# Kernel tuning notes

Measured on AMD Instinct MI355X. Metric: run time of the kernel, lower is better.

Reference implementation:

```python
import jax, jax.numpy as jnp
import numpy as np

FREQ_RES = 100.0 / 256.0
NUM_FILTERS = 6
_CFG = [(0.5, 4.0), (4.0, 8.0), (8.0, 12.0), (12.0, 16.0), (16.0, 24.0), (24.0, 30.0)]
BANDS = [(int(a / FREQ_RES), int(b / FREQ_RES)) for a, b in _CFG]  # (start_bin, end_bin)


def _interp_idx(n_src, n_dst):
    # torch F.interpolate bilinear, align_corners=False, along last dim (T dim is identity since same size)
    j = np.arange(n_dst)
    src = np.maximum((j + 0.5) * n_src / n_dst - 0.5, 0.0)
    x0 = np.floor(src).astype(np.int32)
    x1 = np.minimum(x0 + 1, n_src - 1)
    w = (src - x0).astype(np.float32)
    return x0, x1, w


def _gelu(x):
    return jax.nn.gelu(x, approximate=False)


def _forward(spec, centers, widths, gains, align_w, align_b, fc1_w, fc1_b, fc2_w, fc2_b,
             band_gain, gate_w, gate_b, proj_w, proj_b, bn_gamma, bn_beta, bn_mean, bn_var):
    B, C, T, F = spec.shape
    N = NUM_FILTERS
    band_feats = []
    for i, (s, e) in enumerate(BANDS):
        nb = e - s + 1
        sl = spec[:, :, :, s:e + 1]                       # [B,C,T,nb]
        mu = jax.nn.softplus(centers[i]) + s              # [C,N]
        mu = jnp.clip(mu, s, s + nb - 1)
        std = jnp.clip(jax.nn.softplus(widths[i]) + 1e-3, 0.5, 2.0 * nb / N)
        freqs = jnp.arange(nb, dtype=spec.dtype)          # relative bins [nb]
        g = jnp.exp(-0.5 * ((freqs[None, None, :] - mu[:, :, None]) / std[:, :, None]) ** 2)  # [C,N,nb]
        w = gains[i][:, :, None] * g / (g.sum(-1, keepdims=True) + 1e-6)
        filt = jnp.einsum('bctf,cnf->bctn', sl, w)        # [B,C,T,N]
        aligned = jnp.einsum('bctn,dc->bdtn', filt, align_w[i]) + align_b[i][None, :, None, None]
        band_feats.append(aligned)
    band_stack = jnp.stack(band_feats, axis=1)            # [B,6,C,T,N]
    nb_bands = band_stack.shape[1]
    x = band_stack.reshape(B, nb_bands * C, T, N)
    h = _gelu(jnp.einsum('bktn,ok->botn', x, fc1_w) + fc1_b[None, :, None, None])
    attn = jnp.einsum('botn,ko->bktn', h, fc2_w) + fc2_b[None, :, None, None]
    attn = jax.nn.softmax(attn.reshape(B, nb_bands, C, T, N), axis=1)  # softmax over bands
    band_stack = band_stack * attn * band_gain[None, :, None, None, None]
    enhanced = jnp.zeros_like(spec)
    for i, (s, e) in enumerate(BANDS):
        nb = e - s + 1
        narrow = band_stack[:, i]                         # [B,C,T,N]
        x0, x1, wl = _interp_idx(NUM_FILTERS, nb)
        wl = jnp.asarray(wl, dtype=spec.dtype)
        bf = narrow[..., x0] * (1.0 - wl) + narrow[..., x1] * wl   # [B,C,T,nb]
        enhanced = enhanced.at[:, :, :, s:e + 1].add(bf)
    residual = enhanced - spec
    gate = jax.nn.sigmoid(jnp.einsum('bctf,dc->bdtf', residual, gate_w) + gate_b[None, :, None, None])
    enhanced2 = spec + gate * residual
    y = jnp.einsum('bctf,dc->bdtf', enhanced2, proj_w) + proj_b[None, :, None, None]
    y = (y - bn_mean[None, :, None, None]) / jnp.sqrt(bn_var[None, :, None, None] + 1e-5)
    y = y * bn_gamma[None, :, None, None] + bn_beta[None, :, None, None]
    return _gelu(y)


def setup_inputs() -> dict:
    key = jax.random.key(0)
    ks = jax.random.split(key, 8)
    B, C, T, F, N = 64, 3, 3000, 103, NUM_FILTERS
    spec = jax.random.normal(ks[0], (B, C, T, F), dtype=jnp.float32)
    centers = jnp.stack([jnp.broadcast_to(jnp.linspace(a, b, N, dtype=jnp.float32) / FREQ_RES, (C, N)) for a, b in _CFG])
    widths = jnp.stack([jnp.full((C, N), (b - a) / N / FREQ_RES, dtype=jnp.float32) for a, b in _CFG])
    gains = jnp.ones((6, C, N), jnp.float32)
    align_w = jax.random.normal(ks[1], (6, C, C), dtype=jnp.float32) / np.sqrt(C)
    align_b = jax.random.normal(ks[2], (6, C), dtype=jnp.float32) * 0.02
    inter = 2 * C
    fc1_w = jax.random.normal(ks[3], (inter, 6 * C), dtype=jnp.float32) / np.sqrt(6 * C)
    fc1_b = jnp.zeros((inter,), jnp.float32)
    fc2_w = jax.random.normal(ks[4], (6 * C, inter), dtype=jnp.float32) / np.sqrt(inter)
    fc2_b = jnp.zeros((6 * C,), jnp.float32)
    band_gain = jnp.ones((6,), jnp.float32)
    gate_w = jax.random.normal(ks[5], (C, C), dtype=jnp.float32) / np.sqrt(C)
    gate_b = jnp.zeros((C,), jnp.float32)
    proj_w = jax.random.normal(ks[6], (C, C), dtype=jnp.float32) / np.sqrt(C)
    proj_b = jnp.zeros((C,), jnp.float32)
    bn_gamma = jnp.ones((C,), jnp.float32)
    bn_beta = jnp.zeros((C,), jnp.float32)
    bn_mean = jnp.zeros((C,), jnp.float32)
    bn_var = jnp.ones((C,), jnp.float32)
    return {"spec": spec, "centers": centers, "widths": widths, "gains": gains,
            "align_w": align_w, "align_b": align_b, "fc1_w": fc1_w, "fc1_b": fc1_b,
            "fc2_w": fc2_w, "fc2_b": fc2_b, "band_gain": band_gain,
            "gate_w": gate_w, "gate_b": gate_b, "proj_w": proj_w, "proj_b": proj_b,
            "bn_gamma": bn_gamma, "bn_beta": bn_beta, "bn_mean": bn_mean, "bn_var": bn_var}


def reference(spec, centers, widths, gains, align_w, align_b, fc1_w, fc1_b, fc2_w, fc2_b,
              band_gain, gate_w, gate_b, proj_w, proj_b, bn_gamma, bn_beta, bn_mean, bn_var):
    return _forward(spec, centers, widths, gains, align_w, align_b, fc1_w, fc1_b, fc2_w, fc2_b,
                    band_gain, gate_w, gate_b, proj_w, proj_b, bn_gamma, bn_beta, bn_mean, bn_var)
```

## Files before the change

### kernel.cpp

```cpp
#include <hip/hip_runtime.h>
#include <math.h>

namespace {

constexpr int C_ = 3, T_ = 3000, F_ = 103, NB_ = 6;
constexpr int TT = 20;
constexpr int BS[NB_]  = {1, 10, 20, 30, 40, 61};
constexpr int BNB[NB_] = {10, 11, 11, 11, 22, 16};
constexpr int BOF[NB_] = {0, 10, 21, 32, 43, 65};
constexpr int SPF = 81;
constexpr int PLANE = T_ * F_;
constexpr int SECP = 2064;
constexpr int POOLN = 6320;

__device__ __forceinline__ float softplus_(float x) {
  return fmaxf(x, 0.0f) + log1pf(expf(-fabsf(x)));
}
__device__ __forceinline__ float sigmoid_(float z) {
  return 1.0f / (1.0f + __expf(-z));
}
__device__ __forceinline__ float gelu_(float x) {
  return x * sigmoid_(1.595769122f * x * (1.0f + 0.044715f * x * x));
}

__global__ __launch_bounds__(256)
void sleepband_kernel(const float* __restrict__ spec,
                      const float* __restrict__ centers,
                      const float* __restrict__ widths,
                      const float* __restrict__ gains,
                      const float* __restrict__ align_w,
                      const float* __restrict__ align_b,
                      const float* __restrict__ fc1_w,
                      const float* __restrict__ fc1_b,
                      const float* __restrict__ fc2_w,
                      const float* __restrict__ fc2_b,
                      const float* __restrict__ band_gain,
                      const float* __restrict__ gate_w,
                      const float* __restrict__ gate_b,
                      const float* __restrict__ proj_w,
                      const float* __restrict__ proj_b,
                      const float* __restrict__ bn_gamma,
                      const float* __restrict__ bn_beta,
                      const float* __restrict__ bn_mean,
                      const float* __restrict__ bn_var,
                      float* __restrict__ out)
{
  __shared__ __align__(16) float sPool[POOLN];
  __shared__ float sBand[TT][109];
  __shared__ float sAw[54], sAb[18], sF1[108], sF1b[6], sF2[108], sF2b[18],
                   sBg[6], sGw[9], sGb[3], sPw[9], sPb[3];

  const int tid = threadIdx.x;
  const int t0  = blockIdx.x * TT;
  const int b   = blockIdx.y;

  float* sW = sPool + C_ * TT * SPF;

  const float* specB = spec + (size_t)b * C_ * PLANE;
  for (int li = tid; li < C_ * TT * SPF; li += 256) {
    int c   = li / (TT * SPF);
    int rem = li - c * (TT * SPF);
    int tt  = rem / SPF;
    int f   = rem - tt * SPF;
    sPool[li] = specB[(size_t)c * PLANE + (size_t)(t0 + tt) * F_ + f];
  }

  const float* sp0 = specB + (size_t)t0 * F_;
  const int e1 = tid * 4;
  const int e2 = e1 + 1024;
  const float4 pA1 = *(const float4*)(sp0 + e1);
  const float4 pB1 = *(const float4*)(sp0 + PLANE + e1);
  const float4 pC1 = *(const float4*)(sp0 + 2 * PLANE + e1);
  const float4 pA2 = *(const float4*)(sp0 + e2);
  const float4 pB2 = *(const float4*)(sp0 + PLANE + e2);
  const float4 pC2 = *(const float4*)(sp0 + 2 * PLANE + e2);
  float4 pA3 = {0,0,0,0}, pB3 = {0,0,0,0}, pC3 = {0,0,0,0};
  const int e3 = 2048 + tid * 4;
  if (tid < 3) {
    pA3 = *(const float4*)(sp0 + e3);
    pB3 = *(const float4*)(sp0 + PLANE + e3);
    pC3 = *(const float4*)(sp0 + 2 * PLANE + e3);
  }

  if (tid < 54)  sAw[tid]  = align_w[tid];
  if (tid < 18)  sAb[tid]  = align_b[tid];
  if (tid < 108) sF1[tid]  = fc1_w[tid];
  if (tid < 6)   sF1b[tid] = fc1_b[tid];
  if (tid < 108) sF2[tid]  = fc2_w[tid];
  if (tid < 18)  sF2b[tid] = fc2_b[tid];
  if (tid < 6)   sBg[tid]  = band_gain[tid];
  if (tid < 9)   sGw[tid]  = gate_w[tid];
  if (tid < 3)   sGb[tid]  = gate_b[tid];
  if (tid < 9) {
    int d = tid / 3;
    float sc = bn_gamma[d] / sqrtf(bn_var[d] + 1e-5f);
    sPw[tid] = proj_w[tid] * sc;
  }
  if (tid < 3) {
    float sc = bn_gamma[tid] / sqrtf(bn_var[tid] + 1e-5f);
    sPb[tid] = (proj_b[tid] - bn_mean[tid]) * sc + bn_beta[tid];
  }

  if (tid >= 128 && tid < 128 + 108) {
    int q = tid - 128;
    int i = q / 18;
    int p = q - i * 18;
    int s = BS[i], nb = BNB[i];
    float mu = softplus_(centers[q]) + (float)s;
    mu = fminf(fmaxf(mu, (float)s), (float)(s + nb - 1));
    float sd = softplus_(widths[q]) + 0.001f;
    sd = fminf(fmaxf(sd, 0.5f), 2.0f * (float)nb / 6.0f);
    float sum = 0.0f;
    for (int f = 0; f < nb; ++f) {
      float d = ((float)f - mu) / sd;
      sum += __expf(-0.5f * d * d);
    }
    float sc = gains[q] / (sum + 1e-6f);
    float* wrow = &sW[BOF[i] * 18 + p * nb];
    for (int f = 0; f < nb; ++f) {
      float d = ((float)f - mu) / sd;
      wrow[f] = sc * __expf(-0.5f * d * d);
    }
  }
  __syncthreads();

  for (int task = tid; task < 18 * TT; task += 256) {
    int p  = task / TT;
    int tt = task - p * TT;
    int c  = p / 6;
    int n  = p - c * 6;
    const float* srowb = &sPool[(c * TT + tt) * SPF];
    #pragma unroll
    for (int i = 0; i < NB_; ++i) {
      const float* wrow = &sW[BOF[i] * 18 + p * BNB[i]];
      const float* srow = srowb + BS[i];
      float acc = 0.0f;
      #pragma unroll
      for (int f = 0; f < BNB[i]; ++f) acc += srow[f] * wrow[f];
      sBand[tt][(i * 3 + c) * 6 + n] = acc;
    }
  }
  __syncthreads();

  if (tid < 6 * TT) {
    int n  = tid / TT;
    int tt = tid - n * TT;
    float al[18];
    #pragma unroll
    for (int i = 0; i < 6; ++i) {
      float f0 = sBand[tt][(i * 3 + 0) * 6 + n];
      float f1 = sBand[tt][(i * 3 + 1) * 6 + n];
      float f2 = sBand[tt][(i * 3 + 2) * 6 + n];
      #pragma unroll
      for (int d = 0; d < 3; ++d)
        al[i * 3 + d] = sAw[i * 9 + d * 3 + 0] * f0 + sAw[i * 9 + d * 3 + 1] * f1 +
                        sAw[i * 9 + d * 3 + 2] * f2 + sAb[i * 3 + d];
    }
    float h[6];
    #pragma unroll
    for (int o = 0; o < 6; ++o) {
      float acc = sF1b[o];
      #pragma unroll
      for (int k = 0; k < 18; ++k) acc += sF1[o * 18 + k] * al[k];
      h[o] = gelu_(acc);
    }
    float at[18];
    #pragma unroll
    for (int k = 0; k < 18; ++k) {
      float acc = sF2b[k];
      #pragma unroll
      for (int o = 0; o < 6; ++o) acc += sF2[k * 6 + o] * h[o];
      at[k] = acc;
    }
    #pragma unroll
    for (int c = 0; c < 3; ++c) {
      float m = at[c];
      #pragma unroll
      for (int i = 1; i < 6; ++i) m = fmaxf(m, at[i * 3 + c]);
      float e[6], ssum = 0.0f;
      #pragma unroll
      for (int i = 0; i < 6; ++i) { e[i] = __expf(at[i * 3 + c] - m); ssum += e[i]; }
      float inv = 1.0f / ssum;
      #pragma unroll
      for (int i = 0; i < 6; ++i)
        sBand[tt][(i * 3 + c) * 6 + n] = al[i * 3 + c] * (e[i] * inv) * sBg[i];
    }
  }
  __syncthreads();

  if (tid < C_ * TT) {
    const int c  = tid / TT;
    const int tt = tid - c * TT;
    float bnd[36];
    #pragma unroll
    for (int i = 0; i < 6; ++i)
      #pragma unroll
      for (int n = 0; n < 6; ++n)
        bnd[i * 6 + n] = sBand[tt][(i * 3 + c) * 6 + n];
    float* row = &sPool[c * SECP + tt * F_];
    row[0] = 0.0f;
    float carry = 0.0f;
    #pragma unroll
    for (int i = 0; i < NB_; ++i) {
      #pragma unroll
      for (int j = 0; j < BNB[i]; ++j) {
        float src = ((float)j + 0.5f) * 6.0f / (float)BNB[i] - 0.5f;
        src = src > 0.0f ? src : 0.0f;
        int   x0 = (int)src;
        int   x1 = (x0 < 5) ? x0 + 1 : 5;
        float wl = src - (float)x0;
        float v  = bnd[i * 6 + x0] * (1.0f - wl) + bnd[i * 6 + x1] * wl;
        if (j == 0) v += carry;
        if (i < NB_ - 1 && j == BNB[i] - 1) carry = v;
        else row[BS[i] + j] = v;
      }
    }
    #pragma unroll
    for (int f = 77; f < F_; ++f) row[f] = 0.0f;
  }
  __syncthreads();

  float gw[9], pw[9], gb3[3], pb3[3];
  #pragma unroll
  for (int k = 0; k < 9; ++k) { gw[k] = sGw[k]; pw[k] = sPw[k]; }
  #pragma unroll
  for (int k = 0; k < 3; ++k) { gb3[k] = sGb[k]; pb3[k] = sPb[k]; }

  float* outB = out + (size_t)b * C_ * PLANE + (size_t)t0 * F_;

  auto fin = [&](int e, const float4& sA, const float4& sB, const float4& sC) {
    const float4 eA = *(const float4*)&sPool[0 * SECP + e];
    const float4 eB = *(const float4*)&sPool[1 * SECP + e];
    const float4 eC = *(const float4*)&sPool[2 * SECP + e];
    float4 oA, oB, oC;
    const float* sAp = (const float*)&sA; const float* sBp = (const float*)&sB;
    const float* sCp = (const float*)&sC;
    const float* eAp = (const float*)&eA; const float* eBp = (const float*)&eB;
    const float* eCp = (const float*)&eC;
    float* oAp = (float*)&oA; float* oBp = (float*)&oB; float* oCp = (float*)&oC;
    #pragma unroll
    for (int j = 0; j < 4; ++j) {
      float sv0 = sAp[j], sv1 = sBp[j], sv2 = sCp[j];
      float r0 = eAp[j] - sv0, r1 = eBp[j] - sv1, r2 = eCp[j] - sv2;
      float e20 = sv0 + sigmoid_(gw[0] * r0 + gw[1] * r1 + gw[2] * r2 + gb3[0]) * r0;
      float e21 = sv1 + sigmoid_(gw[3] * r0 + gw[4] * r1 + gw[5] * r2 + gb3[1]) * r1;
      float e22 = sv2 + sigmoid_(gw[6] * r0 + gw[7] * r1 + gw[8] * r2 + gb3[2]) * r2;
      float y0 = pw[0] * e20 + pw[1] * e21 + pw[2] * e22 + pb3[0];
      float y1 = pw[3] * e20 + pw[4] * e21 + pw[5] * e22 + pb3[1];
      float y2 = pw[6] * e20 + pw[7] * e21 + pw[8] * e22 + pb3[2];
      oAp[j] = gelu_(y0); oBp[j] = gelu_(y1); oCp[j] = gelu_(y2);
    }
    *(float4*)(outB + e) = oA;
    *(float4*)(outB + PLANE + e) = oB;
    *(float4*)(outB + 2 * PLANE + e) = oC;
  };

  fin(e1, pA1, pB1, pC1);
  fin(e2, pA2, pB2, pC2);
  if (tid < 3) fin(e3, pA3, pB3, pC3);
}

}

extern "C" void kernel_launch(void* const* d_in, const int* in_sizes, int n_in,
                              void* d_out, int out_size, void* d_ws, size_t ws_size,
                              hipStream_t stream) {
  (void)n_in; (void)out_size; (void)d_ws; (void)ws_size;
  const int B = in_sizes[0] / (C_ * T_ * F_);
  dim3 grid(T_ / TT, B);
  sleepband_kernel<<<grid, 256, 0, stream>>>(
      (const float*)d_in[0],  (const float*)d_in[1],  (const float*)d_in[2],
      (const float*)d_in[3],  (const float*)d_in[4],  (const float*)d_in[5],
      (const float*)d_in[6],  (const float*)d_in[7],  (const float*)d_in[8],
      (const float*)d_in[9],  (const float*)d_in[10], (const float*)d_in[11],
      (const float*)d_in[12], (const float*)d_in[13], (const float*)d_in[14],
      (const float*)d_in[15], (const float*)d_in[16], (const float*)d_in[17],
      (const float*)d_in[18], (float*)d_out);
}
```

Baseline: 254.5 us.

## Cut register pressure: defer spec reloads, coarsen filter and MLP stages, raise occupancy

Drops the early float4 prefetch of the spec tile into registers and instead reloads spec from global memory inside a loop in the final gate/projection stage. This shortens register live ranges across the middle stages. The filter stage now has each thread compute three filter outputs from one shared spectrum read, and the attention MLP stage has each thread process two time steps so shared weight loads are reused. Launch bounds request 4 blocks per CU. The trade-off is that the final stage now waits on a global load that was previously overlapped, and fewer threads are active in the middle stages.

```diff
diff --git a/kernel.cpp b/kernel.cpp
--- a/kernel.cpp
+++ b/kernel.cpp
@@ -23,7 +23,7 @@
   return x * sigmoid_(1.595769122f * x * (1.0f + 0.044715f * x * x));
 }
 
-__global__ __launch_bounds__(256)
+__global__ __launch_bounds__(256, 4)
 void sleepband_kernel(const float* __restrict__ spec,
                       const float* __restrict__ centers,
                       const float* __restrict__ widths,
@@ -65,23 +65,6 @@
     sPool[li] = specB[(size_t)c * PLANE + (size_t)(t0 + tt) * F_ + f];
   }
 
-  const float* sp0 = specB + (size_t)t0 * F_;
-  const int e1 = tid * 4;
-  const int e2 = e1 + 1024;
-  const float4 pA1 = *(const float4*)(sp0 + e1);
-  const float4 pB1 = *(const float4*)(sp0 + PLANE + e1);
-  const float4 pC1 = *(const float4*)(sp0 + 2 * PLANE + e1);
-  const float4 pA2 = *(const float4*)(sp0 + e2);
-  const float4 pB2 = *(const float4*)(sp0 + PLANE + e2);
-  const float4 pC2 = *(const float4*)(sp0 + 2 * PLANE + e2);
-  float4 pA3 = {0,0,0,0}, pB3 = {0,0,0,0}, pC3 = {0,0,0,0};
-  const int e3 = 2048 + tid * 4;
-  if (tid < 3) {
-    pA3 = *(const float4*)(sp0 + e3);
-    pB3 = *(const float4*)(sp0 + PLANE + e3);
-    pC3 = *(const float4*)(sp0 + 2 * PLANE + e3);
-  }
-
   if (tid < 54)  sAw[tid]  = align_w[tid];
   if (tid < 18)  sAb[tid]  = align_b[tid];
   if (tid < 108) sF1[tid]  = fc1_w[tid];
@@ -124,66 +107,102 @@
   }
   __syncthreads();
 
-  for (int task = tid; task < 18 * TT; task += 256) {
-    int p  = task / TT;
-    int tt = task - p * TT;
-    int c  = p / 6;
-    int n  = p - c * 6;
-    const float* srowb = &sPool[(c * TT + tt) * SPF];
-    #pragma unroll
-    for (int i = 0; i < NB_; ++i) {
-      const float* wrow = &sW[BOF[i] * 18 + p * BNB[i]];
-      const float* srow = srowb + BS[i];
-      float acc = 0.0f;
-      #pragma unroll
-      for (int f = 0; f < BNB[i]; ++f) acc += srow[f] * wrow[f];
-      sBand[tt][(i * 3 + c) * 6 + n] = acc;
+  {
+    const int ng  = tid >> 6;
+    const int idx = tid & 63;
+    if (ng < 2 && idx < 60) {
+      const int c  = idx / 20;
+      const int tt = idx - c * 20;
+      const int n0 = ng * 3;
+      const float* srowb = &sPool[(c * TT + tt) * SPF];
+      #pragma unroll
+      for (int i = 0; i < NB_; ++i) {
+        const int nb = BNB[i];
+        const float* w0 = &sW[BOF[i] * 18 + (c * 6 + n0) * nb];
+        const float* sr = srowb + BS[i];
+        float a0 = 0.0f, a1 = 0.0f, a2 = 0.0f;
+        #pragma unroll
+        for (int f = 0; f < nb; ++f) {
+          float s = sr[f];
+          a0 += s * w0[f];
+          a1 += s * w0[nb + f];
+          a2 += s * w0[2 * nb + f];
+        }
+        sBand[tt][(i * 3 + c) * 6 + n0 + 0] = a0;
+        sBand[tt][(i * 3 + c) * 6 + n0 + 1] = a1;
+        sBand[tt][(i * 3 + c) * 6 + n0 + 2] = a2;
+      }
     }
   }
   __syncthreads();
 
-  if (tid < 6 * TT) {
-    int n  = tid / TT;
-    int tt = tid - n * TT;
-    float al[18];
+  if (tid < 60) {
+    const int n   = tid / 10;
+    const int tth = tid - n * 10;
+    const int tA  = 2 * tth, tB = tA + 1;
+    float al0[18], al1[18];
     #pragma unroll
     for (int i = 0; i < 6; ++i) {
-      float f0 = sBand[tt][(i * 3 + 0) * 6 + n];
-      float f1 = sBand[tt][(i * 3 + 1) * 6 + n];
-      float f2 = sBand[tt][(i * 3 + 2) * 6 + n];
-      #pragma unroll
-      for (int d = 0; d < 3; ++d)
-        al[i * 3 + d] = sAw[i * 9 + d * 3 + 0] * f0 + sAw[i * 9 + d * 3 + 1] * f1 +
-                        sAw[i * 9 + d * 3 + 2] * f2 + sAb[i * 3 + d];
-    }
-    float h[6];
+      float f00 = sBand[tA][(i * 3 + 0) * 6 + n];
+      float f01 = sBand[tA][(i * 3 + 1) * 6 + n];
+      float f02 = sBand[tA][(i * 3 + 2) * 6 + n];
+      float f10 = sBand[tB][(i * 3 + 0) * 6 + n];
+      float f11 = sBand[tB][(i * 3 + 1) * 6 + n];
+      float f12 = sBand[tB][(i * 3 + 2) * 6 + n];
+      #pragma unroll
+      for (int d = 0; d < 3; ++d) {
+        float w0 = sAw[i * 9 + d * 3 + 0];
+        float w1 = sAw[i * 9 + d * 3 + 1];
+        float w2 = sAw[i * 9 + d * 3 + 2];
+        float bb = sAb[i * 3 + d];
+        al0[i * 3 + d] = w0 * f00 + w1 * f01 + w2 * f02 + bb;
+        al1[i * 3 + d] = w0 * f10 + w1 * f11 + w2 * f12 + bb;
+      }
+    }
+    float h0[6], h1[6];
     #pragma unroll
     for (int o = 0; o < 6; ++o) {
-      float acc = sF1b[o];
-      #pragma unroll
-      for (int k = 0; k < 18; ++k) acc += sF1[o * 18 + k] * al[k];
-      h[o] = gelu_(acc);
-    }
-    float at[18];
-    #pragma unroll
-    for (int k = 0; k < 18; ++k) {
-      float acc = sF2b[k];
-      #pragma unroll
-      for (int o = 0; o < 6; ++o) acc += sF2[k * 6 + o] * h[o];
-      at[k] = acc;
+      float a0 = sF1b[o], a1 = sF1b[o];
+      #pragma unroll
+      for (int k = 0; k < 18; ++k) {
+        float w = sF1[o * 18 + k];
+        a0 += w * al0[k];
+        a1 += w * al1[k];
+      }
+      h0[o] = gelu_(a0);
+      h1[o] = gelu_(a1);
     }
     #pragma unroll
     for (int c = 0; c < 3; ++c) {
-      float m = at[c];
-      #pragma unroll
-      for (int i = 1; i < 6; ++i) m = fmaxf(m, at[i * 3 + c]);
-      float e[6], ssum = 0.0f;
-      #pragma unroll
-      for (int i = 0; i < 6; ++i) { e[i] = __expf(at[i * 3 + c] - m); ssum += e[i]; }
-      float inv = 1.0f / ssum;
-      #pragma unroll
-      for (int i = 0; i < 6; ++i)
-        sBand[tt][(i * 3 + c) * 6 + n] = al[i * 3 + c] * (e[i] * inv) * sBg[i];
+      float a0[6], a1[6];
+      #pragma unroll
+      for (int i = 0; i < 6; ++i) {
+        const int k = i * 3 + c;
+        float x0 = sF2b[k], x1 = sF2b[k];
+        #pragma unroll
+        for (int o = 0; o < 6; ++o) {
+          float w = sF2[k * 6 + o];
+          x0 += w * h0[o];
+          x1 += w * h1[o];
+        }
+        a0[i] = x0; a1[i] = x1;
+      }
+      float m0 = a0[0], m1 = a1[0];
+      #pragma unroll
+      for (int i = 1; i < 6; ++i) { m0 = fmaxf(m0, a0[i]); m1 = fmaxf(m1, a1[i]); }
+      float e0[6], e1[6], s0 = 0.0f, s1 = 0.0f;
+      #pragma unroll
+      for (int i = 0; i < 6; ++i) {
+        e0[i] = __expf(a0[i] - m0); s0 += e0[i];
+        e1[i] = __expf(a1[i] - m1); s1 += e1[i];
+      }
+      float i0 = 1.0f / s0, i1 = 1.0f / s1;
+      #pragma unroll
+      for (int i = 0; i < 6; ++i) {
+        float bg = sBg[i];
+        sBand[tA][(i * 3 + c) * 6 + n] = al0[i * 3 + c] * (e0[i] * i0) * bg;
+        sBand[tB][(i * 3 + c) * 6 + n] = al1[i * 3 + c] * (e1[i] * i1) * bg;
+      }
     }
   }
   __syncthreads();
@@ -226,9 +245,15 @@
   #pragma unroll
   for (int k = 0; k < 3; ++k) { gb3[k] = sGb[k]; pb3[k] = sPb[k]; }
 
+  const float* sp0 = specB + (size_t)t0 * F_;
   float* outB = out + (size_t)b * C_ * PLANE + (size_t)t0 * F_;
-
-  auto fin = [&](int e, const float4& sA, const float4& sB, const float4& sC) {
+  for (int e4 = tid; e4 < (TT * F_) / 4 + 1; e4 += 256) {
+    if (e4 >= (TT * F_ + 3) / 4) break;
+    const int e = e4 * 4;
+    if (e >= TT * F_) break;
+    const float4 sA = *(const float4*)(sp0 + e);
+    const float4 sB = *(const float4*)(sp0 + PLANE + e);
+    const float4 sC = *(const float4*)(sp0 + 2 * PLANE + e);
     const float4 eA = *(const float4*)&sPool[0 * SECP + e];
     const float4 eB = *(const float4*)&sPool[1 * SECP + e];
     const float4 eC = *(const float4*)&sPool[2 * SECP + e];
@@ -253,11 +278,7 @@
     *(float4*)(outB + e) = oA;
     *(float4*)(outB + PLANE + e) = oB;
     *(float4*)(outB + 2 * PLANE + e) = oC;
-  };
-
-  fin(e1, pA1, pB1, pC1);
-  fin(e2, pA2, pB2, pC2);
-  if (tid < 3) fin(e3, pA3, pB3, pC3);
+  }
 }
 
 }
```

After: 265.7 us. 4.4% more time.

## Hoist filter-weight prep into separate kernel and loop blocks over multiple time tiles

Applied to the files above, without the earlier changes.

Gaussian filter weights and BN-folded projection parameters are now computed once by a small prep kernel into workspace, rather than recomputed by every block. Each main block then handles NT consecutive time tiles in a loop, which amortises the parameter loads over more work and cuts the grid size by NT. The trade-offs are an extra kernel launch, fewer blocks (and so possibly lower occupancy or poor load balance across CUs), and losing the early prefetch of the residual spec values, which are now loaded inside the serialized per-tile loop.

```diff
diff --git a/kernel.cpp b/kernel.cpp
--- a/kernel.cpp
+++ b/kernel.cpp
@@ -5,13 +5,15 @@
 
 constexpr int C_ = 3, T_ = 3000, F_ = 103, NB_ = 6;
 constexpr int TT = 20;
+constexpr int NT = 5;
 constexpr int BS[NB_]  = {1, 10, 20, 30, 40, 61};
 constexpr int BNB[NB_] = {10, 11, 11, 11, 22, 16};
 constexpr int BOF[NB_] = {0, 10, 21, 32, 43, 65};
 constexpr int SPF = 81;
 constexpr int PLANE = T_ * F_;
 constexpr int SECP = 2064;
-constexpr int POOLN = 6320;
+constexpr int WTOT = 1458;
+constexpr int POOL2 = 6192;
 
 __device__ __forceinline__ float softplus_(float x) {
   return fmaxf(x, 0.0f) + log1pf(expf(-fabsf(x)));
@@ -23,86 +25,20 @@
   return x * sigmoid_(1.595769122f * x * (1.0f + 0.044715f * x * x));
 }
 
-__global__ __launch_bounds__(256)
-void sleepband_kernel(const float* __restrict__ spec,
-                      const float* __restrict__ centers,
-                      const float* __restrict__ widths,
-                      const float* __restrict__ gains,
-                      const float* __restrict__ align_w,
-                      const float* __restrict__ align_b,
-                      const float* __restrict__ fc1_w,
-                      const float* __restrict__ fc1_b,
-                      const float* __restrict__ fc2_w,
-                      const float* __restrict__ fc2_b,
-                      const float* __restrict__ band_gain,
-                      const float* __restrict__ gate_w,
-                      const float* __restrict__ gate_b,
-                      const float* __restrict__ proj_w,
-                      const float* __restrict__ proj_b,
-                      const float* __restrict__ bn_gamma,
-                      const float* __restrict__ bn_beta,
-                      const float* __restrict__ bn_mean,
-                      const float* __restrict__ bn_var,
-                      float* __restrict__ out)
+__global__ __launch_bounds__(128)
+void prep_kernel(const float* __restrict__ centers,
+                 const float* __restrict__ widths,
+                 const float* __restrict__ gains,
+                 const float* __restrict__ proj_w,
+                 const float* __restrict__ proj_b,
+                 const float* __restrict__ bn_gamma,
+                 const float* __restrict__ bn_beta,
+                 const float* __restrict__ bn_mean,
+                 const float* __restrict__ bn_var,
+                 float* __restrict__ ws)
 {
-  __shared__ __align__(16) float sPool[POOLN];
-  __shared__ float sBand[TT][109];
-  __shared__ float sAw[54], sAb[18], sF1[108], sF1b[6], sF2[108], sF2b[18],
-                   sBg[6], sGw[9], sGb[3], sPw[9], sPb[3];
-
-  const int tid = threadIdx.x;
-  const int t0  = blockIdx.x * TT;
-  const int b   = blockIdx.y;
-
-  float* sW = sPool + C_ * TT * SPF;
-
-  const float* specB = spec + (size_t)b * C_ * PLANE;
-  for (int li = tid; li < C_ * TT * SPF; li += 256) {
-    int c   = li / (TT * SPF);
-    int rem = li - c * (TT * SPF);
-    int tt  = rem / SPF;
-    int f   = rem - tt * SPF;
-    sPool[li] = specB[(size_t)c * PLANE + (size_t)(t0 + tt) * F_ + f];
-  }
-
-  const float* sp0 = specB + (size_t)t0 * F_;
-  const int e1 = tid * 4;
-  const int e2 = e1 + 1024;
-  const float4 pA1 = *(const float4*)(sp0 + e1);
-  const float4 pB1 = *(const float4*)(sp0 + PLANE + e1);
-  const float4 pC1 = *(const float4*)(sp0 + 2 * PLANE + e1);
-  const float4 pA2 = *(const float4*)(sp0 + e2);
-  const float4 pB2 = *(const float4*)(sp0 + PLANE + e2);
-  const float4 pC2 = *(const float4*)(sp0 + 2 * PLANE + e2);
-  float4 pA3 = {0,0,0,0}, pB3 = {0,0,0,0}, pC3 = {0,0,0,0};
-  const int e3 = 2048 + tid * 4;
-  if (tid < 3) {
-    pA3 = *(const float4*)(sp0 + e3);
-    pB3 = *(const float4*)(sp0 + PLANE + e3);
-    pC3 = *(const float4*)(sp0 + 2 * PLANE + e3);
-  }
-
-  if (tid < 54)  sAw[tid]  = align_w[tid];
-  if (tid < 18)  sAb[tid]  = align_b[tid];
-  if (tid < 108) sF1[tid]  = fc1_w[tid];
-  if (tid < 6)   sF1b[tid] = fc1_b[tid];
-  if (tid < 108) sF2[tid]  = fc2_w[tid];
-  if (tid < 18)  sF2b[tid] = fc2_b[tid];
-  if (tid < 6)   sBg[tid]  = band_gain[tid];
-  if (tid < 9)   sGw[tid]  = gate_w[tid];
-  if (tid < 3)   sGb[tid]  = gate_b[tid];
-  if (tid < 9) {
-    int d = tid / 3;
-    float sc = bn_gamma[d] / sqrtf(bn_var[d] + 1e-5f);
-    sPw[tid] = proj_w[tid] * sc;
-  }
-  if (tid < 3) {
-    float sc = bn_gamma[tid] / sqrtf(bn_var[tid] + 1e-5f);
-    sPb[tid] = (proj_b[tid] - bn_mean[tid]) * sc + bn_beta[tid];
-  }
-
-  if (tid >= 128 && tid < 128 + 108) {
-    int q = tid - 128;
+  const int q = threadIdx.x;
+  if (q < 108) {
     int i = q / 18;
     int p = q - i * 18;
     int s = BS[i], nb = BNB[i];
@@ -116,148 +52,208 @@
       sum += __expf(-0.5f * d * d);
     }
     float sc = gains[q] / (sum + 1e-6f);
-    float* wrow = &sW[BOF[i] * 18 + p * nb];
+    float* wrow = &ws[BOF[i] * 18 + p * nb];
     for (int f = 0; f < nb; ++f) {
       float d = ((float)f - mu) / sd;
       wrow[f] = sc * __expf(-0.5f * d * d);
     }
+  } else if (q < 117) {
+    int k = q - 108, d = k / 3;
+    float sc = bn_gamma[d] / sqrtf(bn_var[d] + 1e-5f);
+    ws[WTOT + k] = proj_w[k] * sc;
+  } else if (q < 120) {
+    int d = q - 117;
+    float sc = bn_gamma[d] / sqrtf(bn_var[d] + 1e-5f);
+    ws[WTOT + 9 + d] = (proj_b[d] - bn_mean[d]) * sc + bn_beta[d];
   }
-  __syncthreads();
-
-  for (int task = tid; task < 18 * TT; task += 256) {
-    int p  = task / TT;
-    int tt = task - p * TT;
-    int c  = p / 6;
-    int n  = p - c * 6;
-    const float* srowb = &sPool[(c * TT + tt) * SPF];
+}
+
+__global__ __launch_bounds__(256)
+void sleepband_kernel(const float* __restrict__ spec,
+                      const float* __restrict__ ws,
+                      const float* __restrict__ align_w,
+                      const float* __restrict__ align_b,
+                      const float* __restrict__ fc1_w,
+                      const float* __restrict__ fc1_b,
+                      const float* __restrict__ fc2_w,
+                      const float* __restrict__ fc2_b,
+                      const float* __restrict__ band_gain,
+                      const float* __restrict__ gate_w,
+                      const float* __restrict__ gate_b,
+                      float* __restrict__ out)
+{
+  __shared__ __align__(16) float sPool[POOL2];
+  __shared__ float sW[WTOT];
+  __shared__ float sBand[TT][109];
+  __shared__ float sAw[54], sAb[18], sF1[108], sF1b[6], sF2[108], sF2b[18],
+                   sBg[6], sGw[9], sGb[3], sPw[9], sPb[3];
+
+  const int tid = threadIdx.x;
+  const int b   = blockIdx.y;
+  const float* specB = spec + (size_t)b * C_ * PLANE;
+  float* outBase = out + (size_t)b * C_ * PLANE;
+
+  for (int k = tid; k < WTOT; k += 256) sW[k] = ws[k];
+  if (tid < 54)  sAw[tid]  = align_w[tid];
+  if (tid < 18)  sAb[tid]  = align_b[tid];
+  if (tid < 108) sF1[tid]  = fc1_w[tid];
+  if (tid < 6)   sF1b[tid] = fc1_b[tid];
+  if (tid < 108) sF2[tid]  = fc2_w[tid];
+  if (tid < 18)  sF2b[tid] = fc2_b[tid];
+  if (tid < 6)   sBg[tid]  = band_gain[tid];
+  if (tid < 9)   sGw[tid]  = gate_w[tid];
+  if (tid < 3)   sGb[tid]  = gate_b[tid];
+  if (tid < 9)   sPw[tid]  = ws[WTOT + tid];
+  if (tid < 3)   sPb[tid]  = ws[WTOT + 9 + tid];
+
+  for (int tile = 0; tile < NT; ++tile) {
+    const int t0 = (blockIdx.x * NT + tile) * TT;
+
+    for (int li = tid; li < C_ * TT * SPF; li += 256) {
+      int c   = li / (TT * SPF);
+      int rem = li - c * (TT * SPF);
+      int tt  = rem / SPF;
+      int f   = rem - tt * SPF;
+      sPool[li] = specB[(size_t)c * PLANE + (size_t)(t0 + tt) * F_ + f];
+    }
+    __syncthreads();
+
+    for (int task = tid; task < 18 * TT; task += 256) {
+      int p  = task / TT;
+      int tt = task - p * TT;
+      int c  = p / 6;
+      int n  = p - c * 6;
+      const float* srowb = &sPool[(c * TT + tt) * SPF];
+      #pragma unroll
+      for (int i = 0; i < NB_; ++i) {
+        const float* wrow = &sW[BOF[i] * 18 + p * BNB[i]];
+        const float* srow = srowb + BS[i];
+        float acc = 0.0f;
+        #pragma unroll
+        for (int f = 0; f < BNB[i]; ++f) acc += srow[f] * wrow[f];
+        sBand[tt][(i * 3 + c) * 6 + n] = acc;
+      }
+    }
+    __syncthreads();
+
+    if (tid < 6 * TT) {
+      int n  = tid / TT;
+      int tt = tid - n * TT;
+      float al[18];
+      #pragma unroll
+      for (int i = 0; i < 6; ++i) {
+        float f0 = sBand[tt][(i * 3 + 0) * 6 + n];
+        float f1 = sBand[tt][(i * 3 + 1) * 6 + n];
+        float f2 = sBand[tt][(i * 3 + 2) * 6 + n];
+        #pragma unroll
+        for (int d = 0; d < 3; ++d)
+          al[i * 3 + d] = sAw[i * 9 + d * 3 + 0] * f0 + sAw[i * 9 + d * 3 + 1] * f1 +
+                          sAw[i * 9 + d * 3 + 2] * f2 + sAb[i * 3 + d];
+      }
+      float h[6];
+      #pragma unroll
+      for (int o = 0; o < 6; ++o) {
+        float acc = sF1b[o];
+        #pragma unroll
+        for (int k = 0; k < 18; ++k) acc += sF1[o * 18 + k] * al[k];
+        h[o] = gelu_(acc);
+      }
+      float at[18];
+      #pragma unroll
+      for (int k = 0; k < 18; ++k) {
+        float acc = sF2b[k];
+        #pragma unroll
+        for (int o = 0; o < 6; ++o) acc += sF2[k * 6 + o] * h[o];
+        at[k] = acc;
+      }
+      #pragma unroll
+      for (int c = 0; c < 3; ++c) {
+        float m = at[c];
+        #pragma unroll
+        for (int i = 1; i < 6; ++i) m = fmaxf(m, at[i * 3 + c]);
+        float e[6], ssum = 0.0f;
+        #pragma unroll
+        for (int i = 0; i < 6; ++i) { e[i] = __expf(at[i * 3 + c] - m); ssum += e[i]; }
+        float inv = 1.0f / ssum;
+        #pragma unroll
+        for (int i = 0; i < 6; ++i)
+          sBand[tt][(i * 3 + c) * 6 + n] = al[i * 3 + c] * (e[i] * inv) * sBg[i];
+      }
+    }
+    __syncthreads();
+
+    if (tid < C_ * TT) {
+      const int c  = tid / TT;
+      const int tt = tid - c * TT;
+      float bnd[36];
+      #pragma unroll
+      for (int i = 0; i < 6; ++i)
+        #pragma unroll
+        for (int n = 0; n < 6; ++n)
+          bnd[i * 6 + n] = sBand[tt][(i * 3 + c) * 6 + n];
+      float* row = &sPool[c * SECP + tt * F_];
+      row[0] = 0.0f;
+      float carry = 0.0f;
+      #pragma unroll
+      for (int i = 0; i < NB_; ++i) {
+        #pragma unroll
+        for (int j = 0; j < BNB[i]; ++j) {
+          float src = ((float)j + 0.5f) * 6.0f / (float)BNB[i] - 0.5f;
+          src = src > 0.0f ? src : 0.0f;
+          int   x0 = (int)src;
+          int   x1 = (x0 < 5) ? x0 + 1 : 5;
+          float wl = src - (float)x0;
+          float v  = bnd[i * 6 + x0] * (1.0f - wl) + bnd[i * 6 + x1] * wl;
+          if (j == 0) v += carry;
+          if (i < NB_ - 1 && j == BNB[i] - 1) carry = v;
+          else row[BS[i] + j] = v;
+        }
+      }
+      #pragma unroll
+      for (int f = 77; f < F_; ++f) row[f] = 0.0f;
+    }
+    __syncthreads();
+
+    float gw[9], pw[9], gb3[3], pb3[3];
     #pragma unroll
-    for (int i = 0; i < NB_; ++i) {
-      const float* wrow = &sW[BOF[i] * 18 + p * BNB[i]];
-      const float* srow = srowb + BS[i];
-      float acc = 0.0f;
-      #pragma unroll
-      for (int f = 0; f < BNB[i]; ++f) acc += srow[f] * wrow[f];
-      sBand[tt][(i * 3 + c) * 6 + n] = acc;
-    }
+    for (int k = 0; k < 9; ++k) { gw[k] = sGw[k]; pw[k] = sPw[k]; }
+    #pragma unroll
+    for (int k = 0; k < 3; ++k) { gb3[k] = sGb[k]; pb3[k] = sPb[k]; }
+
+    const float* sp0 = specB + (size_t)t0 * F_;
+    float* outB = outBase + (size_t)t0 * F_;
+    for (int e4 = tid; e4 < (TT * F_) / 4; e4 += 256) {
+      const int e = e4 * 4;
+      const float4 sA = *(const float4*)(sp0 + e);
+      const float4 sB = *(const float4*)(sp0 + PLANE + e);
+      const float4 sC = *(const float4*)(sp0 + 2 * PLANE + e);
+      const float4 eA = *(const float4*)&sPool[0 * SECP + e];
+      const float4 eB = *(const float4*)&sPool[1 * SECP + e];
+      const float4 eC = *(const float4*)&sPool[2 * SECP + e];
+      float4 oA, oB, oC;
+      const float* sAp = (const float*)&sA; const float* sBp = (const float*)&sB;
+      const float* sCp = (const float*)&sC;
+      const float* eAp = (const float*)&eA; const float* eBp = (const float*)&eB;
+      const float* eCp = (const float*)&eC;
+      float* oAp = (float*)&oA; float* oBp = (float*)&oB; float* oCp = (float*)&oC;
+      #pragma unroll
+      for (int j = 0; j < 4; ++j) {
+        float sv0 = sAp[j], sv1 = sBp[j], sv2 = sCp[j];
+        float r0 = eAp[j] - sv0, r1 = eBp[j] - sv1, r2 = eCp[j] - sv2;
+        float e20 = sv0 + sigmoid_(gw[0] * r0 + gw[1] * r1 + gw[2] * r2 + gb3[0]) * r0;
+        float e21 = sv1 + sigmoid_(gw[3] * r0 + gw[4] * r1 + gw[5] * r2 + gb3[1]) * r1;
+        float e22 = sv2 + sigmoid_(gw[6] * r0 + gw[7] * r1 + gw[8] * r2 + gb3[2]) * r2;
+        float y0 = pw[0] * e20 + pw[1] * e21 + pw[2] * e22 + pb3[0];
+        float y1 = pw[3] * e20 + pw[4] * e21 + pw[5] * e22 + pb3[1];
+        float y2 = pw[6] * e20 + pw[7] * e21 + pw[8] * e22 + pb3[2];
+        oAp[j] = gelu_(y0); oBp[j] = gelu_(y1); oCp[j] = gelu_(y2);
+      }
+      *(float4*)(outB + e) = oA;
+      *(float4*)(outB + PLANE + e) = oB;
+      *(float4*)(outB + 2 * PLANE + e) = oC;
+    }
+    __syncthreads();
   }
-  __syncthreads();
-
-  if (tid < 6 * TT) {
-    int n  = tid / TT;
-    int tt = tid - n * TT;
-    float al[18];
-    #pragma unroll
-    for (int i = 0; i < 6; ++i) {
-      float f0 = sBand[tt][(i * 3 + 0) * 6 + n];
-      float f1 = sBand[tt][(i * 3 + 1) * 6 + n];
-      float f2 = sBand[tt][(i * 3 + 2) * 6 + n];
-      #pragma unroll
-      for (int d = 0; d < 3; ++d)
-        al[i * 3 + d] = sAw[i * 9 + d * 3 + 0] * f0 + sAw[i * 9 + d * 3 + 1] * f1 +
-                        sAw[i * 9 + d * 3 + 2] * f2 + sAb[i * 3 + d];
-    }
-    float h[6];
-    #pragma unroll
-    for (int o = 0; o < 6; ++o) {
-      float acc = sF1b[o];
-      #pragma unroll
-      for (int k = 0; k < 18; ++k) acc += sF1[o * 18 + k] * al[k];
-      h[o] = gelu_(acc);
-    }
-    float at[18];
-    #pragma unroll
-    for (int k = 0; k < 18; ++k) {
-      float acc = sF2b[k];
-      #pragma unroll
-      for (int o = 0; o < 6; ++o) acc += sF2[k * 6 + o] * h[o];
-      at[k] = acc;
-    }
-    #pragma unroll
-    for (int c = 0; c < 3; ++c) {
-      float m = at[c];
-      #pragma unroll
-      for (int i = 1; i < 6; ++i) m = fmaxf(m, at[i * 3 + c]);
-      float e[6], ssum = 0.0f;
-      #pragma unroll
-      for (int i = 0; i < 6; ++i) { e[i] = __expf(at[i * 3 + c] - m); ssum += e[i]; }
-      float inv = 1.0f / ssum;
-      #pragma unroll
-      for (int i = 0; i < 6; ++i)
-        sBand[tt][(i * 3 + c) * 6 + n] = al[i * 3 + c] * (e[i] * inv) * sBg[i];
-    }
-  }
-  __syncthreads();
-
-  if (tid < C_ * TT) {
-    const int c  = tid / TT;
-    const int tt = tid - c * TT;
-    float bnd[36];
-    #pragma unroll
-    for (int i = 0; i < 6; ++i)
-      #pragma unroll
-      for (int n = 0; n < 6; ++n)
-        bnd[i * 6 + n] = sBand[tt][(i * 3 + c) * 6 + n];
-    float* row = &sPool[c * SECP + tt * F_];
-    row[0] = 0.0f;
-    float carry = 0.0f;
-    #pragma unroll
-    for (int i = 0; i < NB_; ++i) {
-      #pragma unroll
-      for (int j = 0; j < BNB[i]; ++j) {
-        float src = ((float)j + 0.5f) * 6.0f / (float)BNB[i] - 0.5f;
-        src = src > 0.0f ? src : 0.0f;
-        int   x0 = (int)src;
-        int   x1 = (x0 < 5) ? x0 + 1 : 5;
-        float wl = src - (float)x0;
-        float v  = bnd[i * 6 + x0] * (1.0f - wl) + bnd[i * 6 + x1] * wl;
-        if (j == 0) v += carry;
-        if (i < NB_ - 1 && j == BNB[i] - 1) carry = v;
-        else row[BS[i] + j] = v;
-      }
-    }
-    #pragma unroll
-    for (int f = 77; f < F_; ++f) row[f] = 0.0f;
-  }
-  __syncthreads();
-
-  float gw[9], pw[9], gb3[3], pb3[3];
-  #pragma unroll
-  for (int k = 0; k < 9; ++k) { gw[k] = sGw[k]; pw[k] = sPw[k]; }
-  #pragma unroll
-  for (int k = 0; k < 3; ++k) { gb3[k] = sGb[k]; pb3[k] = sPb[k]; }
-
-  float* outB = out + (size_t)b * C_ * PLANE + (size_t)t0 * F_;
-
-  auto fin = [&](int e, const float4& sA, const float4& sB, const float4& sC) {
-    const float4 eA = *(const float4*)&sPool[0 * SECP + e];
-    const float4 eB = *(const float4*)&sPool[1 * SECP + e];
-    const float4 eC = *(const float4*)&sPool[2 * SECP + e];
-    float4 oA, oB, oC;
-    const float* sAp = (const float*)&sA; const float* sBp = (const float*)&sB;
-    const float* sCp = (const float*)&sC;
-    const float* eAp = (const float*)&eA; const float* eBp = (const float*)&eB;
-    const float* eCp = (const float*)&eC;
-    float* oAp = (float*)&oA; float* oBp = (float*)&oB; float* oCp = (float*)&oC;
-    #pragma unroll
-    for (int j = 0; j < 4; ++j) {
-      float sv0 = sAp[j], sv1 = sBp[j], sv2 = sCp[j];
-      float r0 = eAp[j] - sv0, r1 = eBp[j] - sv1, r2 = eCp[j] - sv2;
-      float e20 = sv0 + sigmoid_(gw[0] * r0 + gw[1] * r1 + gw[2] * r2 + gb3[0]) * r0;
-      float e21 = sv1 + sigmoid_(gw[3] * r0 + gw[4] * r1 + gw[5] * r2 + gb3[1]) * r1;
-      float e22 = sv2 + sigmoid_(gw[6] * r0 + gw[7] * r1 + gw[8] * r2 + gb3[2]) * r2;
-      float y0 = pw[0] * e20 + pw[1] * e21 + pw[2] * e22 + pb3[0];
-      float y1 = pw[3] * e20 + pw[4] * e21 + pw[5] * e22 + pb3[1];
-      float y2 = pw[6] * e20 + pw[7] * e21 + pw[8] * e22 + pb3[2];
-      oAp[j] = gelu_(y0); oBp[j] = gelu_(y1); oCp[j] = gelu_(y2);
-    }
-    *(float4*)(outB + e) = oA;
-    *(float4*)(outB + PLANE + e) = oB;
-    *(float4*)(outB + 2 * PLANE + e) = oC;
-  };
-
-  fin(e1, pA1, pB1, pC1);
-  fin(e2, pA2, pB2, pC2);
-  if (tid < 3) fin(e3, pA3, pB3, pC3);
 }
 
 }
@@ -265,15 +261,18 @@
 extern "C" void kernel_launch(void* const* d_in, const int* in_sizes, int n_in,
                               void* d_out, int out_size, void* d_ws, size_t ws_size,
                               hipStream_t stream) {
-  (void)n_in; (void)out_size; (void)d_ws; (void)ws_size;
+  (void)n_in; (void)out_size; (void)ws_size;
   const int B = in_sizes[0] / (C_ * T_ * F_);
-  dim3 grid(T_ / TT, B);
+  float* ws = (float*)d_ws;
+  prep_kernel<<<1, 128, 0, stream>>>(
+      (const float*)d_in[1],  (const float*)d_in[2],  (const float*)d_in[3],
+      (const float*)d_in[13], (const float*)d_in[14], (const float*)d_in[15],
+      (const float*)d_in[16], (const float*)d_in[17], (const float*)d_in[18], ws);
+  dim3 grid(T_ / (TT * NT), B);
   sleepband_kernel<<<grid, 256, 0, stream>>>(
-      (const float*)d_in[0],  (const float*)d_in[1],  (const float*)d_in[2],
-      (const float*)d_in[3],  (const float*)d_in[4],  (const float*)d_in[5],
+      (const float*)d_in[0],  ws,
+      (const float*)d_in[4],  (const float*)d_in[5],
       (const float*)d_in[6],  (const float*)d_in[7],  (const float*)d_in[8],
       (const float*)d_in[9],  (const float*)d_in[10], (const float*)d_in[11],
-      (const float*)d_in[12], (const float*)d_in[13], (const float*)d_in[14],
-      (const float*)d_in[15], (const float*)d_in[16], (const float*)d_in[17],
-      (const float*)d_in[18], (float*)d_out);
-}
+      (const float*)d_in[12], (float*)d_out);
+}
```

Measured after the change: 239.1 us. 6.0% less time.
